# Optimization experiments

Hardware: AMD Instinct MI355X
Metric: run time of the kernel (lower is better)

Reference implementation:

```python
import jax, jax.numpy as jnp
import numpy as np

B, S, HID = 2, 2048, 2048
H, HKV, D = 32, 8, 128


def _rope(x, cos, sin):
    # x: [B, S, n_heads, D]; cos/sin: [S, D], only first D//2 columns used.
    half = x.shape[-1] // 2
    x0, x1 = x[..., :half], x[..., half:]
    c = cos[None, :, None, :half]
    s = sin[None, :, None, :half]
    return jnp.concatenate([x0 * c - x1 * s, x0 * s + x1 * c], axis=-1)


def setup_inputs() -> dict:
    key = jax.random.key(0)
    ks = jax.random.split(key, 7)
    return {
        "hidden_states": jax.random.normal(ks[0], (B, S, HID), jnp.float32),
        "sin_table": jax.random.uniform(ks[1], (S, D), jnp.float32),
        "cos_table": jax.random.uniform(ks[2], (S, D), jnp.float32),
        "Wq": jax.random.normal(ks[3], (HID, H * D), jnp.float32) * 0.02,
        "Wk": jax.random.normal(ks[4], (HID, HKV * D), jnp.float32) * 0.02,
        "Wv": jax.random.normal(ks[5], (HID, HKV * D), jnp.float32) * 0.02,
        "Wo": jax.random.normal(ks[6], (H * D, HID), jnp.float32) * 0.02,
    }


def reference(hidden_states, sin_table, cos_table, Wq, Wk, Wv, Wo):
    b, s, _ = hidden_states.shape
    q = (hidden_states @ Wq).reshape(b, s, H, D)
    k = (hidden_states @ Wk).reshape(b, s, HKV, D)
    v = (hidden_states @ Wv).reshape(b, s, HKV, D)

    q = _rope(q, cos_table, sin_table)
    k = _rope(k, cos_table, sin_table)

    q = q.transpose(0, 2, 1, 3)  # [B, H, S, D]
    k = k.transpose(0, 2, 1, 3)  # [B, HKV, S, D]
    v = v.transpose(0, 2, 1, 3)

    g = H // HKV
    k = jnp.repeat(k, g, axis=1)  # [B, H, S, D]
    v = jnp.repeat(v, g, axis=1)

    scale = 1.0 / np.sqrt(D).astype(np.float32)
    scores = jnp.einsum("bhqd,bhkd->bhqk", q, k) * scale
    causal = jnp.tril(jnp.ones((s, s), dtype=bool))
    scores = jnp.where(causal, scores, -jnp.inf)
    attn = jax.nn.softmax(scores, axis=-1)
    out = jnp.einsum("bhqk,bhkd->bhqd", attn, v)  # [B, H, S, D]
    out = out.transpose(0, 2, 1, 3).reshape(b, s, H * D)
    return out @ Wo
```

## Files before the change

### kernel.cpp

```cpp
#include <hip/hip_runtime.h>
#include <hip/hip_bf16.h>
#include <math.h>

#define BB 2
#define SS 2048
#define HID 2048
#define NH 32
#define NKV 8
#define DD 128

typedef unsigned short u16;
typedef __attribute__((ext_vector_type(8))) short short8;
typedef __attribute__((ext_vector_type(4))) float f32x4;
typedef __attribute__((ext_vector_type(16))) float f32x16;
typedef __attribute__((ext_vector_type(4))) unsigned short us4;

__device__ __forceinline__ u16 f2bf(float f) {
    unsigned int u = __float_as_uint(f);
    u += 0x7fff + ((u >> 16) & 1);
    return (u16)(u >> 16);
}
__device__ __forceinline__ float bf2f(u16 h) {
    return __uint_as_float(((unsigned int)h) << 16);
}

#define GLOAD16(gp, lp) __builtin_amdgcn_global_load_lds(                      \
    (const __attribute__((address_space(1))) void*)(gp),                       \
    (__attribute__((address_space(3))) void*)(lp), 16, 0, 0)

#define MFMA32(a, b, c) __builtin_amdgcn_mfma_f32_32x32x16_bf16(a, b, c, 0, 0, 0)

__global__ __launch_bounds__(256) void cvt_k(const float* __restrict__ in,
                                             u16* __restrict__ out, int n8)
{
    int i = blockIdx.x * 256 + threadIdx.x;
    if (i >= n8) return;
    f32x4 a = ((const f32x4*)in)[i * 2];
    f32x4 b = ((const f32x4*)in)[i * 2 + 1];
    short8 o;
#pragma unroll
    for (int j = 0; j < 4; ++j) { o[j] = (short)f2bf(a[j]); o[4 + j] = (short)f2bf(b[j]); }
    ((short8*)out)[i] = o;
}

__global__ __launch_bounds__(256) void tw_k(const float* __restrict__ in,
                                            u16* __restrict__ out, int R, int C)
{
    __shared__ float t[32][33];
    const int tc = blockIdx.x * 32, tr = blockIdx.y * 32;
    const int r = threadIdx.x >> 3, c4 = (threadIdx.x & 7) * 4;
    f32x4 v = *(const f32x4*)(in + (size_t)(tr + r) * C + tc + c4);
#pragma unroll
    for (int j = 0; j < 4; ++j) t[r][c4 + j] = v[j];
    __syncthreads();
    us4 o;
#pragma unroll
    for (int j = 0; j < 4; ++j) o[j] = f2bf(t[c4 + j][r]);
    *(us4*)(out + (size_t)(tc + r) * R + tr + c4) = o;
}

__global__ __launch_bounds__(256) void vtr_k(const u16* __restrict__ Vb,
                                             u16* __restrict__ Vt)
{
    __shared__ u16 t[64][72];
    const int s0 = blockIdx.x * 64, d0 = blockIdx.y * 64;
    const int b = blockIdx.z >> 3, hkv = blockIdx.z & 7;
    const int tid = threadIdx.x;
    const int rr = tid >> 3, cc = (tid & 7) * 8;
#pragma unroll
    for (int it = 0; it < 2; ++it) {
        int row = rr + it * 32;
        short8 v = *(const short8*)(Vb + ((size_t)(b * SS + s0 + row) * NKV + hkv) * DD + d0 + cc);
#pragma unroll
        for (int j = 0; j < 8; ++j) t[row][cc + j] = (u16)v[j];
    }
    __syncthreads();
#pragma unroll
    for (int it = 0; it < 2; ++it) {
        int dr = rr + it * 32;
        short8 o;
#pragma unroll
        for (int j = 0; j < 8; ++j) o[j] = (short)t[cc + j][dr];
        *(short8*)(Vt + ((size_t)(b * NKV + hkv) * DD + d0 + dr) * SS + s0 + cc) = o;
    }
}

__global__ __launch_bounds__(256) void gemmqkv_k(const u16* __restrict__ A,
                                                 const u16* __restrict__ Wcat,
                                                 u16* __restrict__ Qb_,
                                                 u16* __restrict__ Kb_,
                                                 u16* __restrict__ Vb_)
{
    const int K = HID;
    const int swz = (blockIdx.x & 7) * 192 + ((int)blockIdx.x >> 3);
    const int bx = swz % 48, by = swz / 48;
    const int m0 = by * 128, n0 = bx * 128;

    __shared__ u16 Al[128 * 64];
    __shared__ u16 Bl[128 * 64];
    const int tid = threadIdx.x;
    const int lane = tid & 63, w = tid >> 6;
    const int lo = lane & 15, hi = lane >> 4;
    const int wm = w >> 1, wn = w & 1;

    const int srow = w * 32 + (lane >> 3);
    const int sslot = (lane & 7) ^ (lane >> 3);
    const u16* Asrc = A + (size_t)(m0 + srow) * K + sslot * 8;
    const u16* Bsrc = Wcat + (size_t)(n0 + srow) * K + sslot * 8;

    f32x4 acc[4][4] = {};

    for (int k0 = 0; k0 < K; k0 += 64) {
        __syncthreads();
#pragma unroll
        for (int t = 0; t < 4; ++t) {
            GLOAD16(Asrc + (size_t)t * 8 * K + k0, &Al[(w * 32 + t * 8) * 64]);
            GLOAD16(Bsrc + (size_t)t * 8 * K + k0, &Bl[(w * 32 + t * 8) * 64]);
        }
        __syncthreads();
#pragma unroll
        for (int c = 0; c < 2; ++c) {
            short8 af[4], bfv[4];
#pragma unroll
            for (int i = 0; i < 4; ++i) {
                int row = wm * 64 + i * 16 + lo;
                af[i] = *(const short8*)&Al[row * 64 + (((c * 4 + hi) ^ (lo & 7)) * 8)];
            }
#pragma unroll
            for (int j = 0; j < 4; ++j) {
                int row = wn * 64 + j * 16 + lo;
                bfv[j] = *(const short8*)&Bl[row * 64 + (((c * 4 + hi) ^ (lo & 7)) * 8)];
            }
#pragma unroll
            for (int i = 0; i < 4; ++i)
#pragma unroll
                for (int j = 0; j < 4; ++j)
                    acc[i][j] = __builtin_amdgcn_mfma_f32_16x16x32_bf16(af[i], bfv[j], acc[i][j], 0, 0, 0);
        }
    }

    u16* Cb;
    int cstride, cn0;
    if (n0 < 4096)      { Cb = Qb_; cstride = NH * DD;  cn0 = n0; }
    else if (n0 < 5120) { Cb = Kb_; cstride = NKV * DD; cn0 = n0 - 4096; }
    else                { Cb = Vb_; cstride = NKV * DD; cn0 = n0 - 5120; }

#pragma unroll
    for (int i = 0; i < 4; ++i) {
        int gm = m0 + wm * 64 + i * 16 + hi * 4;
#pragma unroll
        for (int j = 0; j < 4; ++j) {
            int gn = cn0 + wn * 64 + j * 16 + lo;
#pragma unroll
            for (int r = 0; r < 4; ++r)
                Cb[(size_t)(gm + r) * cstride + gn] = f2bf(acc[i][j][r]);
        }
    }
}

template<bool C_F32>
__global__ __launch_bounds__(256) void gemm2s_k(const u16* __restrict__ A,
                                                const u16* __restrict__ Bt,
                                                void* __restrict__ Cp,
                                                int M, int N, int K, int nbx)
{
    const int cpx = (int)gridDim.x >> 3;
    const int swz = (blockIdx.x & 7) * cpx + ((int)blockIdx.x >> 3);
    const int bx = swz % nbx, by = swz / nbx;
    const int m0 = by * 128, n0 = bx * 128;

    __shared__ u16 Al[128 * 64];
    __shared__ u16 Bl[128 * 64];
    const int tid = threadIdx.x;
    const int lane = tid & 63, w = tid >> 6;
    const int lo = lane & 15, hi = lane >> 4;
    const int wm = w >> 1, wn = w & 1;

    const int srow = w * 32 + (lane >> 3);
    const int sslot = (lane & 7) ^ (lane >> 3);
    const u16* Asrc = A + (size_t)(m0 + srow) * K + sslot * 8;
    const u16* Bsrc = Bt + (size_t)(n0 + srow) * K + sslot * 8;

    f32x4 acc[4][4] = {};

    for (int k0 = 0; k0 < K; k0 += 64) {
        __syncthreads();
#pragma unroll
        for (int t = 0; t < 4; ++t) {
            GLOAD16(Asrc + (size_t)t * 8 * K + k0, &Al[(w * 32 + t * 8) * 64]);
            GLOAD16(Bsrc + (size_t)t * 8 * K + k0, &Bl[(w * 32 + t * 8) * 64]);
        }
        __syncthreads();
#pragma unroll
        for (int c = 0; c < 2; ++c) {
            short8 af[4], bfv[4];
#pragma unroll
            for (int i = 0; i < 4; ++i) {
                int row = wm * 64 + i * 16 + lo;
                af[i] = *(const short8*)&Al[row * 64 + (((c * 4 + hi) ^ (lo & 7)) * 8)];
            }
#pragma unroll
            for (int j = 0; j < 4; ++j) {
                int row = wn * 64 + j * 16 + lo;
                bfv[j] = *(const short8*)&Bl[row * 64 + (((c * 4 + hi) ^ (lo & 7)) * 8)];
            }
#pragma unroll
            for (int i = 0; i < 4; ++i)
#pragma unroll
                for (int j = 0; j < 4; ++j)
                    acc[i][j] = __builtin_amdgcn_mfma_f32_16x16x32_bf16(af[i], bfv[j], acc[i][j], 0, 0, 0);
        }
    }

#pragma unroll
    for (int i = 0; i < 4; ++i) {
        int gm = m0 + wm * 64 + i * 16 + hi * 4;
#pragma unroll
        for (int j = 0; j < 4; ++j) {
            int gn = n0 + wn * 64 + j * 16 + lo;
#pragma unroll
            for (int r = 0; r < 4; ++r) {
                if constexpr (C_F32)
                    ((float*)Cp)[(size_t)(gm + r) * N + gn] = acc[i][j][r];
                else
                    ((u16*)Cp)[(size_t)(gm + r) * N + gn] = f2bf(acc[i][j][r]);
            }
        }
    }
}

__global__ __launch_bounds__(256) void rope_k(u16* buf,
                                              const float* __restrict__ cosT,
                                              const float* __restrict__ sinT,
                                              int nheads, float scale)
{
    int idx = blockIdx.x * 256 + threadIdx.x;
    int total = BB * SS * nheads * 64;
    if (idx >= total) return;
    int d = idx & 63;
    int rem = idx >> 6;
    int hh = rem % nheads;
    int s = (rem / nheads) & (SS - 1);
    int bb = rem / (nheads * SS);
    size_t base = ((size_t)(bb * SS + s) * nheads + hh) * DD;
    float x0 = bf2f(buf[base + d]), x1 = bf2f(buf[base + d + 64]);
    float c = cosT[s * DD + d], sn = sinT[s * DD + d];
    buf[base + d]      = f2bf((x0 * c - x1 * sn) * scale);
    buf[base + d + 64] = f2bf((x0 * sn + x1 * c) * scale);
}

__device__ __forceinline__ short8 make_pa(float p0, float p1, float p2, float p3,
                                          float p4, float p5, float p6, float p7,
                                          int hi1)
{
    unsigned w0, w1, w2, w3;
    asm("v_cvt_pk_bf16_f32 %0, %1, %2" : "=v"(w0) : "v"(p0), "v"(p1));
    asm("v_cvt_pk_bf16_f32 %0, %1, %2" : "=v"(w1) : "v"(p2), "v"(p3));
    asm("v_cvt_pk_bf16_f32 %0, %1, %2" : "=v"(w2) : "v"(p4), "v"(p5));
    asm("v_cvt_pk_bf16_f32 %0, %1, %2" : "=v"(w3) : "v"(p6), "v"(p7));
    unsigned xw0 = (unsigned)__shfl_xor((int)w0, 32);
    unsigned xw1 = (unsigned)__shfl_xor((int)w1, 32);
    unsigned xw2 = (unsigned)__shfl_xor((int)w2, 32);
    unsigned xw3 = (unsigned)__shfl_xor((int)w3, 32);
    union { unsigned u[4]; short8 s; } cv;
    cv.u[0] = hi1 ? xw2 : w0;
    cv.u[1] = hi1 ? xw3 : w1;
    cv.u[2] = hi1 ? w2 : xw0;
    cv.u[3] = hi1 ? w3 : xw1;
    return cv.s;
}

__global__ __launch_bounds__(256, 2) void attn7_k(const u16* __restrict__ Qb,
                                                  const u16* __restrict__ Kb,
                                                  const u16* __restrict__ Vt,
                                                  u16* __restrict__ AO)
{
    const int wgid = blockIdx.x;
    const int swz = (wgid & 7) * 128 + (wgid >> 3);
    const int qt = 15 - (swz & 15);
    const int h  = (swz >> 4) & 31;
    const int b  = swz >> 9;
    const int hkv = h >> 2;
    const int tid = threadIdx.x;
    const int w = tid >> 6, lane = tid & 63;
    const int l31 = lane & 31, hi1 = lane >> 5;
    const int qr0 = qt * 128 + w * 32;

    __shared__ u16 Kl[2][64 * 128];
    __shared__ u16 Vl[2][128 * 64];

    short8 qf[8];
    {
        const u16* qrow = Qb + ((size_t)(b * SS + qr0 + l31) * NH + h) * DD + hi1 * 8;
#pragma unroll
        for (int ks = 0; ks < 8; ++ks) qf[ks] = *(const short8*)(qrow + ks * 16);
    }

    const u16* kbase = Kb + ((size_t)b * SS * NKV + hkv) * DD;
    const u16* vbase = Vt + (size_t)(b * NKV + hkv) * DD * SS;

    f32x16 oacc[4] = {};
    float mreg = -INFINITY, lreg = 0.f;

    const int nkt = 2 * qt + 2;
    const int rk = lane >> 4, sk = lane & 15;
    const int rv = lane >> 3, sv = lane & 7;

#pragma unroll
    for (int i = 0; i < 4; ++i) {
        const int c = w * 4 + i;
        const int krow = c * 4 + rk;
        GLOAD16(kbase + (size_t)krow * (NKV * DD) + ((sk ^ (krow & 15)) * 8), &Kl[0][c * 512]);
        const int vrow = c * 8 + rv;
        GLOAD16(vbase + (size_t)vrow * SS + ((sv ^ (vrow & 7)) * 8), &Vl[0][c * 512]);
    }
    __syncthreads();

    int buf = 0;
    for (int kt = 0; kt < nkt; ++kt) {
        const int kv0 = kt * 64;
        if (kt + 1 < nkt) {
            const int kv1 = kv0 + 64;
#pragma unroll
            for (int i = 0; i < 4; ++i) {
                const int c = w * 4 + i;
                const int krow = c * 4 + rk;
                GLOAD16(kbase + (size_t)(kv1 + krow) * (NKV * DD) + ((sk ^ (krow & 15)) * 8),
                        &Kl[buf ^ 1][c * 512]);
                const int vrow = c * 8 + rv;
                GLOAD16(vbase + (size_t)vrow * SS + kv1 + ((sv ^ (vrow & 7)) * 8),
                        &Vl[buf ^ 1][c * 512]);
            }
        }

        if (kv0 <= qr0 + 31) {
            const u16* Kc = Kl[buf];
            const u16* Vc = Vl[buf];

            f32x16 s0 = {}, s1 = {};
            __builtin_amdgcn_s_setprio(1);
#pragma unroll
            for (int ks = 0; ks < 8; ++ks) {
                const int slot = (((2 * ks + hi1) ^ sk) * 8);
                short8 kf0 = *(const short8*)&Kc[l31 * 128 + slot];
                s0 = MFMA32(kf0, qf[ks], s0);
                short8 kf1 = *(const short8*)&Kc[(32 + l31) * 128 + slot];
                s1 = MFMA32(kf1, qf[ks], s1);
            }
            __builtin_amdgcn_s_setprio(0);

            const int qab = qr0 + l31;
            if (kv0 + 63 > qr0) {
#pragma unroll
                for (int r = 0; r < 16; ++r) {
                    const int off = (r & 3) + 8 * (r >> 2) + 4 * hi1;
                    if (kv0 + off > qab)      s0[r] = -INFINITY;
                    if (kv0 + 32 + off > qab) s1[r] = -INFINITY;
                }
            }
            float m0 = fmaxf(s0[0], s1[0]), m1 = fmaxf(s0[1], s1[1]);
            float m2 = fmaxf(s0[2], s1[2]), m3 = fmaxf(s0[3], s1[3]);
#pragma unroll
            for (int r = 4; r < 16; r += 4) {
                m0 = fmaxf(m0, fmaxf(s0[r],     s1[r]));
                m1 = fmaxf(m1, fmaxf(s0[r + 1], s1[r + 1]));
                m2 = fmaxf(m2, fmaxf(s0[r + 2], s1[r + 2]));
                m3 = fmaxf(m3, fmaxf(s0[r + 3], s1[r + 3]));
            }
            float mx = fmaxf(fmaxf(m0, m1), fmaxf(m2, m3));
            mx = fmaxf(mx, __shfl_xor(mx, 32));

            if (__any(mx > mreg + 8.0f)) {
                const float nm = fmaxf(mreg, mx);
                const float al = exp2f(mreg - nm);
                mreg = nm;
                lreg *= al;
#pragma unroll
                for (int r = 0; r < 16; ++r) {
                    const float ar = __shfl(al, (r & 3) + 8 * (r >> 2) + 4 * hi1);
#pragma unroll
                    for (int db = 0; db < 4; ++db) oacc[db][r] *= ar;
                }
            }

#pragma unroll
            for (int r = 0; r < 16; ++r) {
                s0[r] = exp2f(s0[r] - mreg);
                s1[r] = exp2f(s1[r] - mreg);
            }
            float sa = 0.f, sb = 0.f, sc_ = 0.f, sd = 0.f;
#pragma unroll
            for (int r = 0; r < 16; r += 4) {
                sa  += s0[r]     + s1[r];
                sb  += s0[r + 1] + s1[r + 1];
                sc_ += s0[r + 2] + s1[r + 2];
                sd  += s0[r + 3] + s1[r + 3];
            }
            lreg += (sa + sb) + (sc_ + sd);

            short8 pa0 = make_pa(s0[0], s0[1], s0[2],  s0[3],  s0[4],  s0[5],  s0[6],  s0[7],  hi1);
            short8 pa1 = make_pa(s0[8], s0[9], s0[10], s0[11], s0[12], s0[13], s0[14], s0[15], hi1);
            short8 pa2 = make_pa(s1[0], s1[1], s1[2],  s1[3],  s1[4],  s1[5],  s1[6],  s1[7],  hi1);
            short8 pa3 = make_pa(s1[8], s1[9], s1[10], s1[11], s1[12], s1[13], s1[14], s1[15], hi1);

            __builtin_amdgcn_s_setprio(1);
#pragma unroll
            for (int db = 0; db < 4; ++db) {
                const int vr = (db * 32 + l31) * 64;
                short8 vf0 = *(const short8*)&Vc[vr + (((0 + hi1) ^ sv) * 8)];
                oacc[db] = MFMA32(pa0, vf0, oacc[db]);
                short8 vf1 = *(const short8*)&Vc[vr + (((2 + hi1) ^ sv) * 8)];
                oacc[db] = MFMA32(pa1, vf1, oacc[db]);
                short8 vf2 = *(const short8*)&Vc[vr + (((4 + hi1) ^ sv) * 8)];
                oacc[db] = MFMA32(pa2, vf2, oacc[db]);
                short8 vf3 = *(const short8*)&Vc[vr + (((6 + hi1) ^ sv) * 8)];
                oacc[db] = MFMA32(pa3, vf3, oacc[db]);
            }
            __builtin_amdgcn_s_setprio(0);
        }
        __syncthreads();
        buf ^= 1;
    }

    const float lf = lreg + __shfl_xor(lreg, 32);
#pragma unroll
    for (int r = 0; r < 16; ++r) {
        const int qrw = (r & 3) + 8 * (r >> 2) + 4 * hi1;
        const float linv = 1.0f / __shfl(lf, qrw);
        u16* orow = AO + ((size_t)(b * SS + qr0 + qrw) * NH + h) * DD + l31;
#pragma unroll
        for (int db = 0; db < 4; ++db)
            orow[db * 32] = f2bf(oacc[db][r] * linv);
    }
}

template<bool A_BF16, bool C_F32>
__global__ __launch_bounds__(256) void gemm_k(const void* __restrict__ Ap,
                                              const float* __restrict__ Bp,
                                              void* __restrict__ Cp,
                                              int M, int N, int K)
{
    __shared__ u16 Asm[128 * 40];
    __shared__ u16 Bsm[128 * 40];
    const int tid  = threadIdx.x;
    const int lane = tid & 63, wid = tid >> 6;
    const int lo = lane & 15, hi = lane >> 4;
    const int wm = wid >> 1, wn = wid & 1;
    const int m0 = blockIdx.y * 128, n0 = blockIdx.x * 128;
    f32x4 acc[4][4] = {};
    const int nkt = K >> 5;
    for (int kt = 0; kt < nkt; ++kt) {
        const int k0 = kt << 5;
        __syncthreads();
        if constexpr (A_BF16) {
            const u16* A = (const u16*)Ap;
#pragma unroll
            for (int it = 0; it < 4; ++it) {
                int f = it * 256 + tid;
                int row = f >> 3, kg = (f & 7) * 4;
                us4 v = *(const us4*)(A + (size_t)(m0 + row) * K + k0 + kg);
#pragma unroll
                for (int j = 0; j < 4; ++j) Asm[row * 40 + kg + j] = v[j];
            }
        } else {
            const float* A = (const float*)Ap;
#pragma unroll
            for (int it = 0; it < 4; ++it) {
                int f = it * 256 + tid;
                int row = f >> 3, kg = (f & 7) * 4;
                f32x4 v = *(const f32x4*)(A + (size_t)(m0 + row) * K + k0 + kg);
#pragma unroll
                for (int j = 0; j < 4; ++j) Asm[row * 40 + kg + j] = f2bf(v[j]);
            }
        }
#pragma unroll
        for (int it = 0; it < 4; ++it) {
            int f = it * 256 + tid;
            int kr = f >> 5, cg = (f & 31) * 4;
            f32x4 v = *(const f32x4*)(Bp + (size_t)(k0 + kr) * N + n0 + cg);
#pragma unroll
            for (int j = 0; j < 4; ++j) Bsm[(cg + j) * 40 + kr] = f2bf(v[j]);
        }
        __syncthreads();
        short8 af[4], bfr[4];
#pragma unroll
        for (int i = 0; i < 4; ++i)
            af[i] = *(const short8*)&Asm[(wm * 64 + i * 16 + lo) * 40 + hi * 8];
#pragma unroll
        for (int j = 0; j < 4; ++j)
            bfr[j] = *(const short8*)&Bsm[(wn * 64 + j * 16 + lo) * 40 + hi * 8];
#pragma unroll
        for (int i = 0; i < 4; ++i)
#pragma unroll
            for (int j = 0; j < 4; ++j)
                acc[i][j] = __builtin_amdgcn_mfma_f32_16x16x32_bf16(af[i], bfr[j], acc[i][j], 0, 0, 0);
    }
#pragma unroll
    for (int i = 0; i < 4; ++i) {
        int gm = m0 + wm * 64 + i * 16 + hi * 4;
#pragma unroll
        for (int j = 0; j < 4; ++j) {
            int gn = n0 + wn * 64 + j * 16 + lo;
#pragma unroll
            for (int r = 0; r < 4; ++r) {
                if constexpr (C_F32)
                    ((float*)Cp)[(size_t)(gm + r) * N + gn] = acc[i][j][r];
                else
                    ((u16*)Cp)[(size_t)(gm + r) * N + gn] = f2bf(acc[i][j][r]);
            }
        }
    }
}

__global__ __launch_bounds__(64) void attn_k(const u16* __restrict__ Qb,
                                             const u16* __restrict__ Kb,
                                             const u16* __restrict__ Vb,
                                             u16* __restrict__ AO)
{
    const int blk = blockIdx.x;
    const int qt = blk & (SS / 16 - 1);
    const int h  = (blk >> 7) & (NH - 1);
    const int b  = blk >> 12;
    const int hkv = h >> 2;
    const int lane = threadIdx.x;
    const int lo = lane & 15, hi = lane >> 4;
    const int qbase = qt * 16;
    __shared__ float sc[16][32];
    __shared__ u16 vt[128 * 40];
    short8 qf[4];
    const u16* qrow = Qb + ((size_t)(b * SS + qbase + lo) * NH + h) * DD;
#pragma unroll
    for (int c = 0; c < 4; ++c) qf[c] = *(const short8*)(qrow + c * 32 + hi * 8);
    f32x4 oacc[8] = {};
    float m[4] = {-INFINITY, -INFINITY, -INFINITY, -INFINITY};
    float l[4] = {0.f, 0.f, 0.f, 0.f};
    const int nkt = (qbase + 16 + 31) >> 5;
    for (int kt = 0; kt < nkt; ++kt) {
        const int kv0 = kt << 5;
        f32x4 s0 = {}, s1 = {};
        const u16* kb0 = Kb + ((size_t)(b * SS + kv0) * NKV + hkv) * DD;
#pragma unroll
        for (int c = 0; c < 4; ++c) {
            short8 k0f = *(const short8*)(kb0 + (size_t)lo * (NKV * DD) + c * 32 + hi * 8);
            short8 k1f = *(const short8*)(kb0 + (size_t)(lo + 16) * (NKV * DD) + c * 32 + hi * 8);
            s0 = __builtin_amdgcn_mfma_f32_16x16x32_bf16(qf[c], k0f, s0, 0, 0, 0);
            s1 = __builtin_amdgcn_mfma_f32_16x16x32_bf16(qf[c], k1f, s1, 0, 0, 0);
        }
#pragma unroll
        for (int i = 0; i < 8; ++i) {
            int g = i * 64 + lane;
            int row = g >> 4, dg = (g & 15) * 8;
            short8 vv = *(const short8*)(Vb + ((size_t)(b * SS + kv0 + row) * NKV + hkv) * DD + dg);
#pragma unroll
            for (int j = 0; j < 8; ++j) vt[(dg + j) * 40 + row] = (u16)vv[j];
        }
        float alpha[4];
#pragma unroll
        for (int r = 0; r < 4; ++r) {
            int qrowi = qbase + hi * 4 + r;
            float v0 = s0[r]; if (kv0 + lo > qrowi)      v0 = -INFINITY;
            float v1 = s1[r]; if (kv0 + 16 + lo > qrowi) v1 = -INFINITY;
            float mx = fmaxf(v0, v1);
#pragma unroll
            for (int off = 1; off < 16; off <<= 1) mx = fmaxf(mx, __shfl_xor(mx, off, 64));
            float nm = fmaxf(m[r], mx);
            float a = __expf(m[r] - nm);
            v0 = __expf(v0 - nm);
            v1 = __expf(v1 - nm);
            float ps = v0 + v1;
#pragma unroll
            for (int off = 1; off < 16; off <<= 1) ps += __shfl_xor(ps, off, 64);
            l[r] = l[r] * a + ps;
            m[r] = nm;
            alpha[r] = a;
            sc[hi * 4 + r][lo] = v0;
            sc[hi * 4 + r][16 + lo] = v1;
        }
#pragma unroll
        for (int n = 0; n < 8; ++n)
#pragma unroll
            for (int r = 0; r < 4; ++r) oacc[n][r] *= alpha[r];
        __syncthreads();
        f32x4 p0 = *(const f32x4*)&sc[lo][hi * 8];
        f32x4 p1 = *(const f32x4*)&sc[lo][hi * 8 + 4];
        short8 pf;
#pragma unroll
        for (int j = 0; j < 4; ++j) {
            pf[j]     = (short)f2bf(p0[j]);
            pf[4 + j] = (short)f2bf(p1[j]);
        }
#pragma unroll
        for (int n = 0; n < 8; ++n) {
            short8 vf = *(const short8*)&vt[(n * 16 + lo) * 40 + hi * 8];
            oacc[n] = __builtin_amdgcn_mfma_f32_16x16x32_bf16(pf, vf, oacc[n], 0, 0, 0);
        }
        __syncthreads();
    }
#pragma unroll
    for (int n = 0; n < 8; ++n) {
#pragma unroll
        for (int r = 0; r < 4; ++r) {
            size_t idx = ((size_t)(b * SS + qbase + hi * 4 + r) * NH + h) * DD + n * 16 + lo;
            AO[idx] = f2bf(oacc[n][r] / l[r]);
        }
    }
}

extern "C" void kernel_launch(void* const* d_in, const int* in_sizes, int n_in,
                              void* d_out, int out_size, void* d_ws, size_t ws_size,
                              hipStream_t stream) {
    const float* hs   = (const float*)d_in[0];
    const float* sinT = (const float*)d_in[1];
    const float* cosT = (const float*)d_in[2];
    const float* Wq   = (const float*)d_in[3];
    const float* Wk   = (const float*)d_in[4];
    const float* Wv   = (const float*)d_in[5];
    const float* Wo   = (const float*)d_in[6];
    float* out = (float*)d_out;
    const int M = BB * SS;
    u16* ws = (u16*)d_ws;

    const size_t NEED = 109051904;
    if (ws_size >= NEED) {
        u16* Qb   = ws;
        u16* Kb   = ws + 16777216;
        u16* Vb   = ws + 20971520;
        u16* Vt   = ws + 25165824;
        u16* Wcat = ws + 29360128;
        u16* hsb  = ws + 41943040;
        u16* Wot  = Wcat;
        u16* AO   = ws + 37748736;

        cvt_k<<<4096, 256, 0, stream>>>(hs, hsb, (M * HID) / 8);
        tw_k<<<dim3(4096 / 32, 2048 / 32), 256, 0, stream>>>(Wq, Wcat, HID, NH * DD);
        tw_k<<<dim3(1024 / 32, 2048 / 32), 256, 0, stream>>>(Wk, Wcat + (size_t)4096 * 2048, HID, NKV * DD);
        tw_k<<<dim3(1024 / 32, 2048 / 32), 256, 0, stream>>>(Wv, Wcat + (size_t)5120 * 2048, HID, NKV * DD);

        gemmqkv_k<<<1536, 256, 0, stream>>>(hsb, Wcat, Qb, Kb, Vb);

        rope_k<<<(BB * SS * NH * 64 + 255) / 256, 256, 0, stream>>>(Qb, cosT, sinT, NH, 0.12751744f);
        rope_k<<<(BB * SS * NKV * 64 + 255) / 256, 256, 0, stream>>>(Kb, cosT, sinT, NKV, 1.0f);
        vtr_k<<<dim3(SS / 64, DD / 64, BB * NKV), 256, 0, stream>>>(Vb, Vt);
        tw_k<<<dim3(2048 / 32, 4096 / 32), 256, 0, stream>>>(Wo, Wot, NH * DD, HID);

        attn7_k<<<SS / 128 * NH * BB, 256, 0, stream>>>(Qb, Kb, Vt, AO);

        gemm2s_k<true><<<512, 256, 0, stream>>>(AO, Wot, out, M, HID, NH * DD, HID / 128);
    } else {
        u16* Qb   = ws;
        u16* Kbuf = Qb   + (size_t)BB * SS * NH * DD;
        u16* Vbuf = Kbuf + (size_t)BB * SS * NKV * DD;
        u16* AO   = Vbuf + (size_t)BB * SS * NKV * DD;

        gemm_k<false, false><<<dim3((NH * DD) / 128, M / 128), 256, 0, stream>>>(hs, Wq, Qb, M, NH * DD, HID);
        gemm_k<false, false><<<dim3((NKV * DD) / 128, M / 128), 256, 0, stream>>>(hs, Wk, Kbuf, M, NKV * DD, HID);
        gemm_k<false, false><<<dim3((NKV * DD) / 128, M / 128), 256, 0, stream>>>(hs, Wv, Vbuf, M, NKV * DD, HID);
        rope_k<<<(BB * SS * NH * 64 + 255) / 256, 256, 0, stream>>>(Qb, cosT, sinT, NH, 0.08838834764831845f);
        rope_k<<<(BB * SS * NKV * 64 + 255) / 256, 256, 0, stream>>>(Kbuf, cosT, sinT, NKV, 1.0f);
        attn_k<<<BB * NH * (SS / 16), 64, 0, stream>>>(Qb, Kbuf, Vbuf, AO);
        gemm_k<true, true><<<dim3(HID / 128, M / 128), 256, 0, stream>>>(AO, Wo, out, M, HID, NH * DD);
    }
}
```

Measured before the change: 405.9 us.

## Fuse V transpose into QKV GEMM epilogue and double attention Q-tile size

The QKV GEMM epilogue now writes V directly in transposed [b,hkv,d,s] layout with 4-element vector stores, removing the separate vtr_k transpose kernel and its round trip through memory. The attention kernel moves to 512-thread blocks covering 256 query rows, so each K/V tile loaded into shared memory is reused by twice as many waves. Blocks are ordered in an interleaved heavy/light pattern to balance causal work. Risks: the transposed V stores are strided (4 contiguous elements each), and the larger blocks with a launch-bounds occupancy hint of 4 may put pressure on registers and shared memory.

```diff
diff --git a/kernel.cpp b/kernel.cpp
--- a/kernel.cpp
+++ b/kernel.cpp
@@ -89,7 +89,7 @@
                                                  const u16* __restrict__ Wcat,
                                                  u16* __restrict__ Qb_,
                                                  u16* __restrict__ Kb_,
-                                                 u16* __restrict__ Vb_)
+                                                 u16* __restrict__ Vt_)
 {
     const int K = HID;
     const int swz = (blockIdx.x & 7) * 192 + ((int)blockIdx.x >> 3);
@@ -139,21 +139,37 @@
         }
     }
 
-    u16* Cb;
-    int cstride, cn0;
-    if (n0 < 4096)      { Cb = Qb_; cstride = NH * DD;  cn0 = n0; }
-    else if (n0 < 5120) { Cb = Kb_; cstride = NKV * DD; cn0 = n0 - 4096; }
-    else                { Cb = Vb_; cstride = NKV * DD; cn0 = n0 - 5120; }
-
-#pragma unroll
-    for (int i = 0; i < 4; ++i) {
-        int gm = m0 + wm * 64 + i * 16 + hi * 4;
-#pragma unroll
-        for (int j = 0; j < 4; ++j) {
-            int gn = cn0 + wn * 64 + j * 16 + lo;
-#pragma unroll
-            for (int r = 0; r < 4; ++r)
-                Cb[(size_t)(gm + r) * cstride + gn] = f2bf(acc[i][j][r]);
+    if (n0 >= 5120) {
+        const int cn0 = n0 - 5120;
+#pragma unroll
+        for (int i = 0; i < 4; ++i) {
+            int gm = m0 + wm * 64 + i * 16 + hi * 4;
+            int bb = gm >> 11, s = gm & (SS - 1);
+#pragma unroll
+            for (int j = 0; j < 4; ++j) {
+                int gn = cn0 + wn * 64 + j * 16 + lo;
+                int hkv = gn >> 7, d = gn & 127;
+                us4 o;
+#pragma unroll
+                for (int r = 0; r < 4; ++r) o[r] = f2bf(acc[i][j][r]);
+                *(us4*)(Vt_ + (((size_t)(bb * NKV + hkv) * DD + d) * SS + s)) = o;
+            }
+        }
+    } else {
+        u16* Cb;
+        int cstride, cn0;
+        if (n0 < 4096) { Cb = Qb_; cstride = NH * DD;  cn0 = n0; }
+        else           { Cb = Kb_; cstride = NKV * DD; cn0 = n0 - 4096; }
+#pragma unroll
+        for (int i = 0; i < 4; ++i) {
+            int gm = m0 + wm * 64 + i * 16 + hi * 4;
+#pragma unroll
+            for (int j = 0; j < 4; ++j) {
+                int gn = cn0 + wn * 64 + j * 16 + lo;
+#pragma unroll
+                for (int r = 0; r < 4; ++r)
+                    Cb[(size_t)(gm + r) * cstride + gn] = f2bf(acc[i][j][r]);
+            }
         }
     }
 }
@@ -270,21 +286,22 @@
     return cv.s;
 }
 
-__global__ __launch_bounds__(256, 2) void attn7_k(const u16* __restrict__ Qb,
+__global__ __launch_bounds__(512, 4) void attn8_k(const u16* __restrict__ Qb,
                                                   const u16* __restrict__ Kb,
                                                   const u16* __restrict__ Vt,
                                                   u16* __restrict__ AO)
 {
     const int wgid = blockIdx.x;
-    const int swz = (wgid & 7) * 128 + (wgid >> 3);
-    const int qt = 15 - (swz & 15);
-    const int h  = (swz >> 4) & 31;
-    const int b  = swz >> 9;
+    const int swz = (wgid & 7) * 64 + (wgid >> 3);
+    const int t = swz & 7;
+    const int qt = (t & 1) ? (t >> 1) : (7 - (t >> 1));
+    const int h  = (swz >> 3) & 31;
+    const int b  = swz >> 8;
     const int hkv = h >> 2;
     const int tid = threadIdx.x;
     const int w = tid >> 6, lane = tid & 63;
     const int l31 = lane & 31, hi1 = lane >> 5;
-    const int qr0 = qt * 128 + w * 32;
+    const int qr0 = qt * 256 + w * 32;
 
     __shared__ u16 Kl[2][64 * 128];
     __shared__ u16 Vl[2][128 * 64];
@@ -302,13 +319,13 @@
     f32x16 oacc[4] = {};
     float mreg = -INFINITY, lreg = 0.f;
 
-    const int nkt = 2 * qt + 2;
+    const int nkt = 4 * qt + 4;
     const int rk = lane >> 4, sk = lane & 15;
     const int rv = lane >> 3, sv = lane & 7;
 
 #pragma unroll
-    for (int i = 0; i < 4; ++i) {
-        const int c = w * 4 + i;
+    for (int i = 0; i < 2; ++i) {
+        const int c = w * 2 + i;
         const int krow = c * 4 + rk;
         GLOAD16(kbase + (size_t)krow * (NKV * DD) + ((sk ^ (krow & 15)) * 8), &Kl[0][c * 512]);
         const int vrow = c * 8 + rv;
@@ -322,8 +339,8 @@
         if (kt + 1 < nkt) {
             const int kv1 = kv0 + 64;
 #pragma unroll
-            for (int i = 0; i < 4; ++i) {
-                const int c = w * 4 + i;
+            for (int i = 0; i < 2; ++i) {
+                const int c = w * 2 + i;
                 const int krow = c * 4 + rk;
                 GLOAD16(kbase + (size_t)(kv1 + krow) * (NKV * DD) + ((sk ^ (krow & 15)) * 8),
                         &Kl[buf ^ 1][c * 512]);
@@ -624,7 +641,6 @@
     if (ws_size >= NEED) {
         u16* Qb   = ws;
         u16* Kb   = ws + 16777216;
-        u16* Vb   = ws + 20971520;
         u16* Vt   = ws + 25165824;
         u16* Wcat = ws + 29360128;
         u16* hsb  = ws + 41943040;
@@ -636,14 +652,13 @@
         tw_k<<<dim3(1024 / 32, 2048 / 32), 256, 0, stream>>>(Wk, Wcat + (size_t)4096 * 2048, HID, NKV * DD);
         tw_k<<<dim3(1024 / 32, 2048 / 32), 256, 0, stream>>>(Wv, Wcat + (size_t)5120 * 2048, HID, NKV * DD);
 
-        gemmqkv_k<<<1536, 256, 0, stream>>>(hsb, Wcat, Qb, Kb, Vb);
+        gemmqkv_k<<<1536, 256, 0, stream>>>(hsb, Wcat, Qb, Kb, Vt);
 
         rope_k<<<(BB * SS * NH * 64 + 255) / 256, 256, 0, stream>>>(Qb, cosT, sinT, NH, 0.12751744f);
         rope_k<<<(BB * SS * NKV * 64 + 255) / 256, 256, 0, stream>>>(Kb, cosT, sinT, NKV, 1.0f);
-        vtr_k<<<dim3(SS / 64, DD / 64, BB * NKV), 256, 0, stream>>>(Vb, Vt);
         tw_k<<<dim3(2048 / 32, 4096 / 32), 256, 0, stream>>>(Wo, Wot, NH * DD, HID);
 
-        attn7_k<<<SS / 128 * NH * BB, 256, 0, stream>>>(Qb, Kb, Vt, AO);
+        attn8_k<<<SS / 256 * NH * BB, 512, 0, stream>>>(Qb, Kb, Vt, AO);
 
         gemm2s_k<true><<<512, 256, 0, stream>>>(AO, Wot, out, M, HID, NH * DD, HID / 128);
     } else {
```

After: 520.0 us. +28.1%, slower.
